# Kernel tuning notes

Hardware: AMD Instinct MI355X
Metric: run time of the kernel (lower is better)

## Reference

```python
import jax, jax.numpy as jnp
import numpy as np
import math

B, C, IMG, P = 32, 3, 224, 16
E, DEPTH, H, MLP = 768, 12, 12, 3072
NP = (IMG // P) ** 2          # 196 patches
S = NP + 1                    # 197 tokens with cls
NCLS = 10
HD = E // H                   # 64 head dim
EPS = 1e-5


def setup_inputs() -> dict:
    key = jax.random.key(0)
    ks = iter(jax.random.split(key, 64))
    n = lambda shape, s=0.02: (jax.random.normal(next(ks), shape, jnp.float32) * s)
    inp = {
        "x": jax.random.normal(next(ks), (B, C, IMG, IMG), jnp.float32),
        "conv_w": n((E, C, P, P)),
        "conv_b": jnp.zeros((E,), jnp.float32),
        "cls_token": n((1, 1, E)),
        "pos_embed": n((1, S, E)),
        # stacked per-layer params, leading dim DEPTH; linear weights stored [in, out]
        "ln1_w": jnp.ones((DEPTH, E), jnp.float32),
        "ln1_b": jnp.zeros((DEPTH, E), jnp.float32),
        "qkv_w": n((DEPTH, E, 3 * E)),
        "qkv_b": jnp.zeros((DEPTH, 3 * E), jnp.float32),
        "proj_w": n((DEPTH, E, E)),
        "proj_b": jnp.zeros((DEPTH, E), jnp.float32),
        "ln2_w": jnp.ones((DEPTH, E), jnp.float32),
        "ln2_b": jnp.zeros((DEPTH, E), jnp.float32),
        "mlp_w1": n((DEPTH, E, MLP)),
        "mlp_b1": jnp.zeros((DEPTH, MLP), jnp.float32),
        "mlp_w2": n((DEPTH, MLP, E)),
        "mlp_b2": jnp.zeros((DEPTH, E), jnp.float32),
        "lnf_w": jnp.ones((E,), jnp.float32),
        "lnf_b": jnp.zeros((E,), jnp.float32),
        "head_w": n((E, NCLS)),
        "head_b": jnp.zeros((NCLS,), jnp.float32),
    }
    return inp


def layernorm(x, w, b):
    mu = jnp.mean(x, axis=-1, keepdims=True)
    var = jnp.mean(jnp.square(x - mu), axis=-1, keepdims=True)
    return (x - mu) * jax.lax.rsqrt(var + EPS) * w + b


def reference(x, conv_w, conv_b, cls_token, pos_embed,
              ln1_w, ln1_b, qkv_w, qkv_b, proj_w, proj_b,
              ln2_w, ln2_b, mlp_w1, mlp_b1, mlp_w2, mlp_b2,
              lnf_w, lnf_b, head_w, head_b):
    # --- patch embedding: stride-P, kernel-P conv == patchify + matmul ---
    g = IMG // P  # 14
    patches = x.reshape(B, C, g, P, g, P).transpose(0, 2, 4, 1, 3, 5).reshape(B, NP, C * P * P)
    wp = conv_w.reshape(E, C * P * P)
    tok = jnp.einsum('bpd,ed->bpe', patches, wp) + conv_b  # [B, NP, E]

    # cls token + positional embedding (dropout = identity at eval)
    h = jnp.concatenate([jnp.broadcast_to(cls_token, (B, 1, E)), tok], axis=1) + pos_embed

    scale = math.sqrt(HD)
    for i in range(DEPTH):
        # --- attention ---
        y = layernorm(h, ln1_w[i], ln1_b[i])
        qkv = (y @ qkv_w[i] + qkv_b[i]).reshape(B, S, 3, H, HD)
        q, k, v = qkv[:, :, 0], qkv[:, :, 1], qkv[:, :, 2]  # [B, S, H, HD]
        attn = jnp.einsum('bqhd,bkhd->bhqk', q, k) / scale
        attn = jax.nn.softmax(attn, axis=-1)
        o = jnp.einsum('bhqk,bkhd->bqhd', attn, v).reshape(B, S, E)
        h = h + (o @ proj_w[i] + proj_b[i])
        # --- MLP ---
        y = layernorm(h, ln2_w[i], ln2_b[i])
        y = jax.nn.gelu(y @ mlp_w1[i] + mlp_b1[i], approximate=False)
        h = h + (y @ mlp_w2[i] + mlp_b2[i])

    h = layernorm(h, lnf_w, lnf_b)
    return h[:, 0] @ head_w + head_b  # [B, NCLS]
```

## Files before the change

### kernel.cpp

```cpp
#include <hip/hip_runtime.h>


typedef __attribute__((ext_vector_type(8))) short short8;
typedef __attribute__((ext_vector_type(8))) unsigned short ushort8;
typedef __attribute__((ext_vector_type(4))) float f32x4;
typedef unsigned short u16;

#define DEV __device__ __forceinline__

DEV u16 f2bf(float f) {
  unsigned int u = __builtin_bit_cast(unsigned int, f);
  u += 0x7fffu + ((u >> 16) & 1u);
  return (u16)(u >> 16);
}
DEV float wred_sum(float v) {
  for (int o = 32; o; o >>= 1) v += __shfl_xor(v, o, 64);
  return v;
}
DEV void glds16(const void* gp, void* lp) {
  __builtin_amdgcn_global_load_lds(
      (const __attribute__((address_space(1))) void*)gp,
      (__attribute__((address_space(3))) void*)lp, 16, 0, 0);
}
DEV int xcd_swz(int flat, int nwg) {
  int q = nwg >> 3, r = nwg & 7;
  int x = flat & 7, o = flat >> 3;
  return (x < r ? x * (q + 1) : r * (q + 1) + (x - r) * q) + o;
}

__global__ __launch_bounds__(256) void cvt4_k(const float* __restrict__ s,
                                              u16* __restrict__ d, long n4) {
  long i = (long)blockIdx.x * 256 + threadIdx.x;
  if (i >= n4) return;
  float4 v = ((const float4*)s)[i];
  ushort4 o;
  o.x = f2bf(v.x); o.y = f2bf(v.y); o.z = f2bf(v.z); o.w = f2bf(v.w);
  ((ushort4*)d)[i] = o;
}

__global__ __launch_bounds__(256) void tpose_k(const float* __restrict__ s,
                                               u16* __restrict__ d, int K,
                                               int N) {
  __shared__ float t[32][33];
  const int bx = blockIdx.x;
  const int by = blockIdx.y;
  const size_t base = (size_t)blockIdx.z * K * N;
  const int c = threadIdx.x & 31, r0 = threadIdx.x >> 5;
#pragma unroll
  for (int i = 0; i < 4; ++i) {
    int r = r0 + i * 8;
    t[r][c] = s[base + (size_t)(by * 32 + r) * N + bx * 32 + c];
  }
  __syncthreads();
#pragma unroll
  for (int i = 0; i < 4; ++i) {
    int r = r0 + i * 8;
    d[base + (size_t)(bx * 32 + r) * K + by * 32 + c] = f2bf(t[c][r]);
  }
}

__global__ __launch_bounds__(256) void patch_k(const float* __restrict__ x,
                                               u16* __restrict__ pt) {
  int i = blockIdx.x * 256 + threadIdx.x;
  int d = i % 768;
  int bp = i / 768;
  int p = bp % 196, b = bp / 196;
  int c = d >> 8, pd = d & 255;
  int py = pd >> 4, px = pd & 15;
  int gy = p / 14, gx = p - gy * 14;
  size_t src = ((size_t)(b * 3 + c) * 224 + gy * 16 + py) * 224 + gx * 16 + px;
  pt[i] = f2bf(x[src]);
}

__global__ __launch_bounds__(256) void clspos_k(const float* __restrict__ cls,
                                                const float* __restrict__ pos,
                                                float* __restrict__ h) {
  int i = blockIdx.x * 256 + threadIdx.x;
  int b = i / 768, e = i - b * 768;
  h[(size_t)b * 197 * 768 + e] = cls[e] + pos[e];
}

template <int EPI>
DEV void epi_store(float v, int grow, int gcol, u16* outb, int ldo,
                   float* outf, const float* pos) {
  if constexpr (EPI == 0) {
    outb[(size_t)grow * ldo + gcol] = f2bf(v);
  } else if constexpr (EPI == 1) {
    float u = __expf(-1.5957691216f * (v + 0.044715f * v * v * v));
    outb[(size_t)grow * ldo + gcol] = f2bf(v / (1.f + u));
  } else if constexpr (EPI == 2) {
    outf[(size_t)grow * ldo + gcol] += v;
  } else {
    int b = grow / 196, p = grow - b * 196;
    outf[(size_t)(grow + b + 1) * 768 + gcol] =
        v + pos[(size_t)(p + 1) * 768 + gcol];
  }
}

template <int EPI>
__global__ __launch_bounds__(512) void gemmK64(
    const u16* __restrict__ A, int lda, const u16* __restrict__ Bt, int ldb,
    const float* __restrict__ bias, u16* __restrict__ outb, int ldo,
    float* __restrict__ outf, const float* __restrict__ pos, int M, int N,
    int K) {
  __shared__ __align__(16) u16 Ak[2][128 * 64];
  __shared__ __align__(16) u16 Bk[2][128 * 64];
  const int tid = threadIdx.x;
  const int lane = tid & 63, wid = tid >> 6;
  const int wm = wid >> 2, wn = wid & 3;
  const int lg = lane >> 4, lr = lane & 15;
  const int nwg = gridDim.x * gridDim.y;
  const int wg = xcd_swz(blockIdx.y * gridDim.x + blockIdx.x, nwg);
  const int tn = wg % gridDim.x, tm = wg / gridDim.x;

  const int r8 = lane >> 3, c8 = lane & 7;
  const int swc = (c8 ^ r8) << 3;
  const u16* aS = A + (size_t)(tm * 128 + wid * 16 + r8) * lda + swc;
  const u16* bS = Bt + (size_t)(tn * 128 + wid * 16 + r8) * ldb + swc;

  auto stage = [&](int buf, int kt) {
    const u16* ak = aS + kt * 64;
    const u16* bk = bS + kt * 64;
    u16* ad = &Ak[buf][wid * 1024];
    u16* bd = &Bk[buf][wid * 1024];
    glds16(ak, ad);
    glds16(ak + (size_t)8 * lda, ad + 512);
    glds16(bk, bd);
    glds16(bk + (size_t)8 * ldb, bd + 512);
  };

  f32x4 acc[4][2] = {};
  auto compute = [&](int buf) {
#pragma unroll
    for (int ks = 0; ks < 2; ++ks) {
      const int pc = (ks << 2) | lg;
      const int po = ((pc ^ (lr & 7)) << 3);
      short8 af[4], bf2[2];
#pragma unroll
      for (int i = 0; i < 4; ++i)
        af[i] = *(const short8*)(&Ak[buf][(wm * 64 + i * 16 + lr) * 64 + po]);
#pragma unroll
      for (int i = 0; i < 2; ++i)
        bf2[i] = *(const short8*)(&Bk[buf][(wn * 32 + i * 16 + lr) * 64 + po]);
#pragma unroll
      for (int mi = 0; mi < 4; ++mi)
#pragma unroll
        for (int ni = 0; ni < 2; ++ni)
          acc[mi][ni] = __builtin_amdgcn_mfma_f32_16x16x32_bf16(
              af[mi], bf2[ni], acc[mi][ni], 0, 0, 0);
    }
  };

  const int nk = K >> 6;
  int cur = 0;
  stage(0, 0);
  __syncthreads();
  for (int kt = 0; kt < nk - 1; ++kt) {
    stage(cur ^ 1, kt + 1);
    compute(cur);
    __syncthreads();
    cur ^= 1;
  }
  compute(cur);

#pragma unroll
  for (int mi = 0; mi < 4; ++mi)
#pragma unroll
    for (int ni = 0; ni < 2; ++ni)
#pragma unroll
      for (int r = 0; r < 4; ++r) {
        int grow = tm * 128 + wm * 64 + mi * 16 + lg * 4 + r;
        int gcol = tn * 128 + wn * 32 + ni * 16 + lr;
        if (grow < M)
          epi_store<EPI>(acc[mi][ni][r] + bias[gcol], grow, gcol, outb, ldo,
                         outf, pos);
      }
}

template <int EPI>
__global__ __launch_bounds__(512) void gemmW2(
    const u16* __restrict__ A, int lda, const u16* __restrict__ Bt, int ldb,
    const float* __restrict__ bias, u16* __restrict__ outb, int ldo,
    float* __restrict__ outf, int M, int K) {
  __shared__ __align__(16) u16 Ak[2][128 * 32];
  __shared__ __align__(16) u16 Bk[2][256 * 32];
  const int tid = threadIdx.x;
  const int lane = tid & 63, wid = tid >> 6;
  const int wm = wid >> 2, wn = wid & 3;
  const int lg = lane >> 4, lr = lane & 15;
  const int nwg = gridDim.x * gridDim.y;
  const int wg = xcd_swz(blockIdx.y * gridDim.x + blockIdx.x, nwg);
  const int tn = wg % gridDim.x, tm = wg / gridDim.x;
  const size_t koff = (EPI == 4) ? (size_t)blockIdx.z * K : 0;

  const int sr = lane >> 2;
  const int sc4 = (((lane & 3) ^ ((lane >> 3) & 3)) << 3);
  const u16* aSrc = A + (size_t)(tm * 128 + wid * 16 + sr) * lda + koff + sc4;
  const u16* bSrc = Bt + (size_t)(tn * 256 + wid * 32 + sr) * ldb + koff + sc4;
  const size_t bRow16 = (size_t)16 * ldb;

  auto stage = [&](int buf, int kt) {
    const u16* ak = aSrc + kt * 32;
    const u16* bk = bSrc + kt * 32;
    glds16(ak, &Ak[buf][wid * 16 * 32]);
    u16* bd = &Bk[buf][wid * 32 * 32];
    glds16(bk, bd);
    glds16(bk + bRow16, bd + 512);
  };

  const int rp = (lg ^ ((lr >> 1) & 3)) << 3;
  f32x4 acc[4][4] = {};
  auto compute = [&](int buf) {
    short8 af[4], bf[4];
#pragma unroll
    for (int i = 0; i < 4; ++i)
      af[i] = *(const short8*)(&Ak[buf][(wm * 64 + i * 16 + lr) * 32 + rp]);
#pragma unroll
    for (int i = 0; i < 4; ++i)
      bf[i] = *(const short8*)(&Bk[buf][(wn * 64 + i * 16 + lr) * 32 + rp]);
#pragma unroll
    for (int mi = 0; mi < 4; ++mi)
#pragma unroll
      for (int ni = 0; ni < 4; ++ni)
        acc[mi][ni] = __builtin_amdgcn_mfma_f32_16x16x32_bf16(
            af[mi], bf[ni], acc[mi][ni], 0, 0, 0);
  };

  const int nk = K >> 5;
  int cur = 0;
  stage(0, 0);
  __syncthreads();
  for (int kt = 0; kt < nk - 1; ++kt) {
    stage(cur ^ 1, kt + 1);
    compute(cur);
    __syncthreads();
    cur ^= 1;
  }
  compute(cur);

#pragma unroll
  for (int mi = 0; mi < 4; ++mi)
#pragma unroll
    for (int ni = 0; ni < 4; ++ni)
#pragma unroll
      for (int r = 0; r < 4; ++r) {
        int grow = tm * 128 + wm * 64 + mi * 16 + lg * 4 + r;
        int gcol = tn * 256 + wn * 64 + ni * 16 + lr;
        if (grow < M) {
          if constexpr (EPI == 4) {
            outf[(size_t)blockIdx.z * M * ldo + (size_t)grow * ldo + gcol] =
                acc[mi][ni][r];
          } else {
            epi_store<EPI>(acc[mi][ni][r] + bias[gcol], grow, gcol, outb, ldo,
                           outf, nullptr);
          }
        }
      }
}

__global__ __launch_bounds__(256) void redK(const float* __restrict__ Cp,
                                            const float* __restrict__ bias,
                                            float* __restrict__ h) {
  size_t i = ((size_t)blockIdx.x * 256 + threadIdx.x) * 4;
  float4 p0 = *(const float4*)(Cp + i);
  float4 p1 = *(const float4*)(Cp + 6304ull * 768 + i);
  float4 p2 = *(const float4*)(Cp + 2ull * 6304 * 768 + i);
  float4 hv = *(const float4*)(h + i);
  float4 bv = *(const float4*)(bias + (int)(i % 768));
  hv.x += p0.x + p1.x + p2.x + bv.x;
  hv.y += p0.y + p1.y + p2.y + bv.y;
  hv.z += p0.z + p1.z + p2.z + bv.z;
  hv.w += p0.w + p1.w + p2.w + bv.w;
  *(float4*)(h + i) = hv;
}

__global__ __launch_bounds__(256) void redln_k(
    const float* __restrict__ Cp, const float* __restrict__ bias,
    float* __restrict__ h, const float* __restrict__ lnw,
    const float* __restrict__ lnb, u16* __restrict__ y) {
  const int lane = threadIdx.x & 63, wv = threadIdx.x >> 6;
  const int r = blockIdx.x * 4 + wv;
  const size_t base = (size_t)r * 768;
  float4 a[3];
  float s = 0.f, q = 0.f;
#pragma unroll
  for (int i = 0; i < 3; ++i) {
    const int off = i * 256 + lane * 4;
    float4 hv = *(const float4*)(h + base + off);
    float4 p0 = *(const float4*)(Cp + base + off);
    float4 p1 = *(const float4*)(Cp + 6304ull * 768 + base + off);
    float4 p2 = *(const float4*)(Cp + 2ull * 6304 * 768 + base + off);
    float4 bv = *(const float4*)(bias + off);
    a[i].x = hv.x + p0.x + p1.x + p2.x + bv.x;
    a[i].y = hv.y + p0.y + p1.y + p2.y + bv.y;
    a[i].z = hv.z + p0.z + p1.z + p2.z + bv.z;
    a[i].w = hv.w + p0.w + p1.w + p2.w + bv.w;
    s += a[i].x + a[i].y + a[i].z + a[i].w;
    q += a[i].x * a[i].x + a[i].y * a[i].y + a[i].z * a[i].z +
         a[i].w * a[i].w;
  }
  s = wred_sum(s);
  q = wred_sum(q);
  float mu = s * (1.f / 768.f);
  float var = q * (1.f / 768.f) - mu * mu;
  float rs = rsqrtf(var + 1e-5f);
#pragma unroll
  for (int i = 0; i < 3; ++i) {
    const int off = i * 256 + lane * 4;
    *(float4*)(h + base + off) = a[i];
    float4 wv4 = *(const float4*)(lnw + off);
    float4 bv4 = *(const float4*)(lnb + off);
    ushort4 o;
    o.x = f2bf((a[i].x - mu) * rs * wv4.x + bv4.x);
    o.y = f2bf((a[i].y - mu) * rs * wv4.y + bv4.y);
    o.z = f2bf((a[i].z - mu) * rs * wv4.z + bv4.z);
    o.w = f2bf((a[i].w - mu) * rs * wv4.w + bv4.w);
    *(ushort4*)(y + base + off) = o;
  }
}

template <int EPI, int BM>
__global__ __launch_bounds__(256) void gemmP(
    const u16* __restrict__ A, int lda, const u16* __restrict__ Bt, int ldb,
    const float* __restrict__ bias, u16* __restrict__ outb, int ldo,
    float* __restrict__ outf, const float* __restrict__ pos, int M, int N,
    int K) {
  constexpr int MI = BM / 32;
  __shared__ __align__(16) u16 Ak[2][BM * 32];
  __shared__ __align__(16) u16 Bk[2][128 * 32];
  const int tid = threadIdx.x;
  const int lane = tid & 63, wid = tid >> 6;
  const int wm = wid >> 1, wn = wid & 1;
  const int lg = lane >> 4, lr = lane & 15;
  const int nwg = gridDim.x * gridDim.y;
  const int wg = xcd_swz(blockIdx.y * gridDim.x + blockIdx.x, nwg);
  const int tn = wg % gridDim.x, tm = wg / gridDim.x;

  const int sr = lane >> 2;
  const int sc4 = (((lane & 3) ^ ((lane >> 3) & 3)) << 3);
  const u16* aSrc = A + (size_t)(tm * BM + wid * (BM / 4) + sr) * lda + sc4;
  const u16* bSrc = Bt + (size_t)(tn * 128 + wid * 32 + sr) * ldb + sc4;
  const size_t aRow16 = (size_t)16 * lda, bRow16 = (size_t)16 * ldb;

  auto stage = [&](int buf, int kt) {
    const u16* ak = aSrc + kt * 32;
    const u16* bk = bSrc + kt * 32;
    u16* ad = &Ak[buf][wid * (BM / 4) * 32];
    u16* bd = &Bk[buf][wid * 1024];
    glds16(ak, ad);
    if constexpr (BM == 128) glds16(ak + aRow16, ad + 512);
    glds16(bk, bd);
    glds16(bk + bRow16, bd + 512);
  };

  const int rp = (lg ^ ((lr >> 1) & 3)) << 3;
  f32x4 acc[MI][4] = {};
  auto compute = [&](int buf) {
    short8 af[MI], bfr[4];
#pragma unroll
    for (int i = 0; i < MI; ++i)
      af[i] =
          *(const short8*)(&Ak[buf][(wm * (BM / 2) + i * 16 + lr) * 32 + rp]);
#pragma unroll
    for (int i = 0; i < 4; ++i)
      bfr[i] = *(const short8*)(&Bk[buf][(wn * 64 + i * 16 + lr) * 32 + rp]);
#pragma unroll
    for (int mi = 0; mi < MI; ++mi)
#pragma unroll
      for (int ni = 0; ni < 4; ++ni)
        acc[mi][ni] = __builtin_amdgcn_mfma_f32_16x16x32_bf16(
            af[mi], bfr[ni], acc[mi][ni], 0, 0, 0);
  };

  const int nk = K >> 5;
  int cur = 0;
  stage(0, 0);
  __syncthreads();
  for (int kt = 0; kt < nk - 1; ++kt) {
    stage(cur ^ 1, kt + 1);
    compute(cur);
    __syncthreads();
    cur ^= 1;
  }
  compute(cur);

#pragma unroll
  for (int mi = 0; mi < MI; ++mi)
#pragma unroll
    for (int ni = 0; ni < 4; ++ni)
#pragma unroll
      for (int r = 0; r < 4; ++r) {
        int grow = tm * BM + wm * (BM / 2) + mi * 16 + lg * 4 + r;
        int gcol = tn * 128 + wn * 64 + ni * 16 + lr;
        if (grow < M)
          epi_store<EPI>(acc[mi][ni][r] + bias[gcol], grow, gcol, outb, ldo,
                         outf, pos);
      }
}

__global__ __launch_bounds__(64) void qksm_k(const u16* __restrict__ qkv,
                                             u16* __restrict__ P) {
  const int bh = blockIdx.x;
  const int qt = blockIdx.y;
  const int lane = threadIdx.x;
  const int lg = lane >> 4, lr = lane & 15;
  const int b = bh / 12, hh = bh - b * 12;
  const u16* base = qkv + (size_t)b * 197 * 2304 + hh * 64;
  int qrow = qt * 16 + lr;
  if (qrow > 196) qrow = 196;
  const u16* qp = base + (size_t)qrow * 2304 + lg * 8;
  short8 a0 = *(const short8*)(qp);
  short8 a1 = *(const short8*)(qp + 32);
  f32x4 c[13];
  const bool kval[2] = {true, (12 * 16 + lr) <= 196};
#pragma unroll
  for (int kt = 0; kt < 13; ++kt) {
    int krow = kt * 16 + lr;
    if (krow > 196) krow = 196;
    const u16* kp = base + 768 + (size_t)krow * 2304 + lg * 8;
    short8 b0 = *(const short8*)(kp);
    short8 b1 = *(const short8*)(kp + 32);
    f32x4 t = {0.f, 0.f, 0.f, 0.f};
    t = __builtin_amdgcn_mfma_f32_16x16x32_bf16(a0, b0, t, 0, 0, 0);
    c[kt] = __builtin_amdgcn_mfma_f32_16x16x32_bf16(a1, b1, t, 0, 0, 0);
  }
  float mr[4], sr_[4];
#pragma unroll
  for (int r = 0; r < 4; ++r) {
    float mm = -3.4e38f;
#pragma unroll
    for (int kt = 0; kt < 13; ++kt)
      if (kval[kt == 12]) mm = fmaxf(mm, c[kt][r] * 0.125f);
#pragma unroll
    for (int o = 1; o < 16; o <<= 1) mm = fmaxf(mm, __shfl_xor(mm, o, 64));
    mr[r] = mm;
  }
#pragma unroll
  for (int r = 0; r < 4; ++r) {
    float s = 0.f;
#pragma unroll
    for (int kt = 0; kt < 13; ++kt) {
      float e = kval[kt == 12] ? __expf(c[kt][r] * 0.125f - mr[r]) : 0.f;
      c[kt][r] = e;
      s += e;
    }
#pragma unroll
    for (int o = 1; o < 16; o <<= 1) s += __shfl_xor(s, o, 64);
    sr_[r] = 1.0f / s;
  }
  u16* pb = P + (size_t)bh * 197 * 224;
#pragma unroll
  for (int r = 0; r < 4; ++r) {
    int q = qt * 16 + lg * 4 + r;
    if (q < 197) {
#pragma unroll
      for (int kt = 0; kt < 13; ++kt)
        pb[(size_t)q * 224 + kt * 16 + lr] = f2bf(c[kt][r] * sr_[r]);
      pb[(size_t)q * 224 + 208 + lr] = 0;
    }
  }
}

__global__ __launch_bounds__(256) void pv_k(const u16* __restrict__ qkv,
                                            const u16* __restrict__ P,
                                            u16* __restrict__ o) {
  __shared__ __align__(16) u16 Vs[224 * 64];
  const int bh = blockIdx.x;
  const int b = bh / 12, hh = bh - b * 12;
  const int tid = threadIdx.x;
  const int lane = tid & 63, ct = tid >> 6;
  const int lg = lane >> 4, lr = lane & 15;
  const u16* vhead = qkv + (size_t)b * 197 * 2304 + 1536 + hh * 64;
#pragma unroll
  for (int it = 0; it < 7; ++it) {
    const int c0 = it * 256 + ct * 64;
    const int c = c0 + lane;
    int row = c >> 3;
    if (row > 196) row = 196;
    glds16(vhead + (size_t)row * 2304 + (c & 7) * 8, &Vs[c0 * 8]);
  }
  __syncthreads();
  short8 vf[7];
#pragma unroll
  for (int ks = 0; ks < 7; ++ks) {
    ushort8 t;
#pragma unroll
    for (int j = 0; j < 8; ++j) {
      int kk = ks * 32 + lg * 8 + j;
      t[j] = Vs[kk * 64 + ct * 16 + lr];
    }
    vf[ks] = __builtin_bit_cast(short8, t);
  }
  const u16* pbase = P + (size_t)bh * 197 * 224;
  u16* ob = o + (size_t)b * 197 * 768 + hh * 64 + ct * 16;
  for (int qt = 0; qt < 13; ++qt) {
    int q = qt * 16 + lr;
    if (q > 196) q = 196;
    const u16* pp = pbase + (size_t)q * 224 + lg * 8;
    f32x4 acc = {0.f, 0.f, 0.f, 0.f};
#pragma unroll
    for (int ks = 0; ks < 7; ++ks) {
      short8 af = *(const short8*)(pp + ks * 32);
      acc = __builtin_amdgcn_mfma_f32_16x16x32_bf16(af, vf[ks], acc, 0, 0, 0);
    }
#pragma unroll
    for (int r = 0; r < 4; ++r) {
      int qq = qt * 16 + lg * 4 + r;
      if (qq < 197) ob[(size_t)qq * 768 + lr] = f2bf(acc[r]);
    }
  }
}

__global__ __launch_bounds__(256) void ln_k(const float* __restrict__ x,
                                            const float* __restrict__ w,
                                            const float* __restrict__ bb,
                                            u16* __restrict__ y) {
  const int lane = threadIdx.x & 63, wv = threadIdx.x >> 6;
  const int r = blockIdx.x * 4 + wv;
  const float* xr = x + (size_t)r * 768;
  float4 v[3];
  float s = 0.f, q = 0.f;
#pragma unroll
  for (int i = 0; i < 3; ++i) {
    v[i] = *(const float4*)(xr + i * 256 + lane * 4);
    s += v[i].x + v[i].y + v[i].z + v[i].w;
    q += v[i].x * v[i].x + v[i].y * v[i].y + v[i].z * v[i].z +
         v[i].w * v[i].w;
  }
  s = wred_sum(s);
  q = wred_sum(q);
  float mu = s * (1.f / 768.f);
  float var = q * (1.f / 768.f) - mu * mu;
  float rs = rsqrtf(var + 1e-5f);
  u16* yr = y + (size_t)r * 768;
#pragma unroll
  for (int i = 0; i < 3; ++i) {
    float4 wv4 = *(const float4*)(w + i * 256 + lane * 4);
    float4 bv4 = *(const float4*)(bb + i * 256 + lane * 4);
    ushort4 o;
    o.x = f2bf((v[i].x - mu) * rs * wv4.x + bv4.x);
    o.y = f2bf((v[i].y - mu) * rs * wv4.y + bv4.y);
    o.z = f2bf((v[i].z - mu) * rs * wv4.z + bv4.z);
    o.w = f2bf((v[i].w - mu) * rs * wv4.w + bv4.w);
    *(ushort4*)(yr + i * 256 + lane * 4) = o;
  }
}

__global__ __launch_bounds__(256) void head_k(
    const float* __restrict__ h, const float* __restrict__ lnw,
    const float* __restrict__ lnb, const float* __restrict__ hw,
    const float* __restrict__ hb, float* __restrict__ out) {
  const int b = blockIdx.x, tid = threadIdx.x;
  const float* xr = h + (size_t)b * 197 * 768;
  float v0 = xr[tid], v1 = xr[tid + 256], v2 = xr[tid + 512];
  float s = v0 + v1 + v2;
  float q = v0 * v0 + v1 * v1 + v2 * v2;
  s = wred_sum(s);
  q = wred_sum(q);
  __shared__ float ss[4], qs[4];
  int lane = tid & 63, wid = tid >> 6;
  if (lane == 0) { ss[wid] = s; qs[wid] = q; }
  __syncthreads();
  float S = ss[0] + ss[1] + ss[2] + ss[3];
  float Q = qs[0] + qs[1] + qs[2] + qs[3];
  float mu = S * (1.f / 768.f);
  float var = Q * (1.f / 768.f) - mu * mu;
  float rs = rsqrtf(var + 1e-5f);
  __shared__ float yb[768];
  yb[tid] = (v0 - mu) * rs * lnw[tid] + lnb[tid];
  yb[tid + 256] = (v1 - mu) * rs * lnw[tid + 256] + lnb[tid + 256];
  yb[tid + 512] = (v2 - mu) * rs * lnw[tid + 512] + lnb[tid + 512];
  __syncthreads();
  float p[10] = {};
  for (int e = tid; e < 768; e += 256) {
    float yv = yb[e];
#pragma unroll
    for (int n = 0; n < 10; ++n) p[n] += yv * hw[(size_t)e * 10 + n];
  }
#pragma unroll
  for (int n = 0; n < 10; ++n) p[n] = wred_sum(p[n]);
  __shared__ float red[4][10];
  if (lane == 0)
#pragma unroll
    for (int n = 0; n < 10; ++n) red[wid][n] = p[n];
  __syncthreads();
  if (tid < 10)
    out[b * 10 + tid] =
        red[0][tid] + red[1][tid] + red[2][tid] + red[3][tid] + hb[tid];
}

extern "C" void kernel_launch(void* const* d_in, const int* in_sizes, int n_in,
                              void* d_out, int out_size, void* d_ws,
                              size_t ws_size, hipStream_t stream) {
  const float* x = (const float*)d_in[0];
  const float* conv_w = (const float*)d_in[1];
  const float* conv_b = (const float*)d_in[2];
  const float* cls = (const float*)d_in[3];
  const float* pos = (const float*)d_in[4];
  const float* ln1w = (const float*)d_in[5];
  const float* ln1b = (const float*)d_in[6];
  const float* qkvw = (const float*)d_in[7];
  const float* qkvbias = (const float*)d_in[8];
  const float* projw = (const float*)d_in[9];
  const float* projb = (const float*)d_in[10];
  const float* ln2w = (const float*)d_in[11];
  const float* ln2b = (const float*)d_in[12];
  const float* w1f = (const float*)d_in[13];
  const float* b1 = (const float*)d_in[14];
  const float* w2f = (const float*)d_in[15];
  const float* b2 = (const float*)d_in[16];
  const float* lnfw = (const float*)d_in[17];
  const float* lnfb = (const float*)d_in[18];
  const float* headw = (const float*)d_in[19];
  const float* headb = (const float*)d_in[20];
  float* out = (float*)d_out;

  char* p = (char*)d_ws;
  auto take = [&](size_t bytes) {
    char* q = p;
    p += (bytes + 255) & ~(size_t)255;
    return q;
  };
  u16* wq = (u16*)take(12ull * 768 * 2304 * 2);
  u16* wpj = (u16*)take(12ull * 768 * 768 * 2);
  u16* w1 = (u16*)take(12ull * 768 * 3072 * 2);
  u16* w2 = (u16*)take(12ull * 3072 * 768 * 2);
  u16* wc = (u16*)take(768ull * 768 * 2);
  float* h = (float*)take(6304ull * 768 * 4);
  u16* y = (u16*)take(6400ull * 768 * 2);
  u16* qkv = (u16*)take(6400ull * 2304 * 2);
  u16* ob = (u16*)take(6400ull * 768 * 2);
  u16* mlpb = (u16*)take(6400ull * 3072 * 2);
  u16* P = (u16*)take(384ull * 197 * 224 * 2);
  float* skP = (float*)take(3ull * 6304 * 768 * 4);
  (void)ws_size; (void)in_sizes; (void)n_in; (void)out_size;

  tpose_k<<<dim3(72, 24, 12), 256, 0, stream>>>(qkvw, wq, 768, 2304);
  tpose_k<<<dim3(24, 24, 12), 256, 0, stream>>>(projw, wpj, 768, 768);
  tpose_k<<<dim3(96, 24, 12), 256, 0, stream>>>(w1f, w1, 768, 3072);
  tpose_k<<<dim3(24, 96, 12), 256, 0, stream>>>(w2f, w2, 3072, 768);
  cvt4_k<<<576, 256, 0, stream>>>(conv_w, wc, 768 * 768 / 4);

  patch_k<<<6272 * 768 / 256, 256, 0, stream>>>(x, mlpb);
  gemmP<3, 64><<<dim3(6, 98), 256, 0, stream>>>(mlpb, 768, wc, 768, conv_b,
                                                nullptr, 0, h, pos, 6272, 768,
                                                768);
  clspos_k<<<32 * 768 / 256, 256, 0, stream>>>(cls, pos, h);

  ln_k<<<1576, 256, 0, stream>>>(h, ln1w, ln1b, y);
  for (int i = 0; i < 12; ++i) {
    gemmW2<0><<<dim3(9, 50), 512, 0, stream>>>(
        y, 768, wq + (size_t)i * 768 * 2304, 768, qkvbias + i * 2304, qkv,
        2304, nullptr, 6304, 768);
    qksm_k<<<dim3(384, 13), 64, 0, stream>>>(qkv, P);
    pv_k<<<384, 256, 0, stream>>>(qkv, P, ob);
    gemmP<2, 64><<<dim3(6, 99), 256, 0, stream>>>(
        ob, 768, wpj + (size_t)i * 768 * 768, 768, projb + i * 768, nullptr,
        768, h, nullptr, 6304, 768, 768);
    ln_k<<<1576, 256, 0, stream>>>(h, ln2w + i * 768, ln2b + i * 768, y);
    gemmK64<1><<<dim3(24, 50), 512, 0, stream>>>(
        y, 768, w1 + (size_t)i * 768 * 3072, 768, b1 + i * 3072, mlpb, 3072,
        nullptr, nullptr, 6304, 3072, 768);
    gemmW2<4><<<dim3(3, 50, 3), 512, 0, stream>>>(
        mlpb, 3072, w2 + (size_t)i * 3072 * 768, 3072, nullptr, nullptr, 768,
        skP, 6304, 1024);
    if (i < 11) {
      redln_k<<<1576, 256, 0, stream>>>(skP, b2 + i * 768, h,
                                        ln1w + (i + 1) * 768,
                                        ln1b + (i + 1) * 768, y);
    } else {
      redK<<<4728, 256, 0, stream>>>(skP, b2 + i * 768, h);
    }
  }

  head_k<<<32, 256, 0, stream>>>(h, lnfw, lnfb, headw, headb, out);
}
```

Before: 2.951 ms.

## Store split-K partials in bf16 and share K tile in LDS for QK softmax

The MLP down-projection split-K partial sums are now written as bf16 instead of fp32, and the reduction and LayerNorm kernels convert them back. This halves the traffic of the partial buffer, at the cost of bf16 rounding on each partial before the residual add. Separately, the QK-softmax kernel now uses one 256-thread block per batch-head. That block loads K into swizzled LDS once and loops its four waves over the query tiles, instead of every 64-thread block reloading K from global memory.

```diff
diff --git a/kernel.cpp b/kernel.cpp
--- a/kernel.cpp
+++ b/kernel.cpp
@@ -12,6 +12,9 @@
   unsigned int u = __builtin_bit_cast(unsigned int, f);
   u += 0x7fffu + ((u >> 16) & 1u);
   return (u16)(u >> 16);
+}
+DEV float bf2f(u16 v) {
+  return __builtin_bit_cast(float, (unsigned int)v << 16);
 }
 DEV float wred_sum(float v) {
   for (int o = 32; o; o >>= 1) v += __shfl_xor(v, o, 64);
@@ -248,8 +251,8 @@
         int gcol = tn * 256 + wn * 64 + ni * 16 + lr;
         if (grow < M) {
           if constexpr (EPI == 4) {
-            outf[(size_t)blockIdx.z * M * ldo + (size_t)grow * ldo + gcol] =
-                acc[mi][ni][r];
+            outb[(size_t)blockIdx.z * M * ldo + (size_t)grow * ldo + gcol] =
+                f2bf(acc[mi][ni][r]);
           } else {
             epi_store<EPI>(acc[mi][ni][r] + bias[gcol], grow, gcol, outb, ldo,
                            outf, nullptr);
@@ -258,24 +261,24 @@
       }
 }
 
-__global__ __launch_bounds__(256) void redK(const float* __restrict__ Cp,
+__global__ __launch_bounds__(256) void redK(const u16* __restrict__ Cp,
                                             const float* __restrict__ bias,
                                             float* __restrict__ h) {
   size_t i = ((size_t)blockIdx.x * 256 + threadIdx.x) * 4;
-  float4 p0 = *(const float4*)(Cp + i);
-  float4 p1 = *(const float4*)(Cp + 6304ull * 768 + i);
-  float4 p2 = *(const float4*)(Cp + 2ull * 6304 * 768 + i);
+  ushort4 q0 = *(const ushort4*)(Cp + i);
+  ushort4 q1 = *(const ushort4*)(Cp + 6304ull * 768 + i);
+  ushort4 q2 = *(const ushort4*)(Cp + 2ull * 6304 * 768 + i);
   float4 hv = *(const float4*)(h + i);
   float4 bv = *(const float4*)(bias + (int)(i % 768));
-  hv.x += p0.x + p1.x + p2.x + bv.x;
-  hv.y += p0.y + p1.y + p2.y + bv.y;
-  hv.z += p0.z + p1.z + p2.z + bv.z;
-  hv.w += p0.w + p1.w + p2.w + bv.w;
+  hv.x += bf2f(q0.x) + bf2f(q1.x) + bf2f(q2.x) + bv.x;
+  hv.y += bf2f(q0.y) + bf2f(q1.y) + bf2f(q2.y) + bv.y;
+  hv.z += bf2f(q0.z) + bf2f(q1.z) + bf2f(q2.z) + bv.z;
+  hv.w += bf2f(q0.w) + bf2f(q1.w) + bf2f(q2.w) + bv.w;
   *(float4*)(h + i) = hv;
 }
 
 __global__ __launch_bounds__(256) void redln_k(
-    const float* __restrict__ Cp, const float* __restrict__ bias,
+    const u16* __restrict__ Cp, const float* __restrict__ bias,
     float* __restrict__ h, const float* __restrict__ lnw,
     const float* __restrict__ lnb, u16* __restrict__ y) {
   const int lane = threadIdx.x & 63, wv = threadIdx.x >> 6;
@@ -287,14 +290,14 @@
   for (int i = 0; i < 3; ++i) {
     const int off = i * 256 + lane * 4;
     float4 hv = *(const float4*)(h + base + off);
-    float4 p0 = *(const float4*)(Cp + base + off);
-    float4 p1 = *(const float4*)(Cp + 6304ull * 768 + base + off);
-    float4 p2 = *(const float4*)(Cp + 2ull * 6304 * 768 + base + off);
+    ushort4 q0 = *(const ushort4*)(Cp + base + off);
+    ushort4 q1 = *(const ushort4*)(Cp + 6304ull * 768 + base + off);
+    ushort4 q2 = *(const ushort4*)(Cp + 2ull * 6304 * 768 + base + off);
     float4 bv = *(const float4*)(bias + off);
-    a[i].x = hv.x + p0.x + p1.x + p2.x + bv.x;
-    a[i].y = hv.y + p0.y + p1.y + p2.y + bv.y;
-    a[i].z = hv.z + p0.z + p1.z + p2.z + bv.z;
-    a[i].w = hv.w + p0.w + p1.w + p2.w + bv.w;
+    a[i].x = hv.x + bf2f(q0.x) + bf2f(q1.x) + bf2f(q2.x) + bv.x;
+    a[i].y = hv.y + bf2f(q0.y) + bf2f(q1.y) + bf2f(q2.y) + bv.y;
+    a[i].z = hv.z + bf2f(q0.z) + bf2f(q1.z) + bf2f(q2.z) + bv.z;
+    a[i].w = hv.w + bf2f(q0.w) + bf2f(q1.w) + bf2f(q2.w) + bv.w;
     s += a[i].x + a[i].y + a[i].z + a[i].w;
     q += a[i].x * a[i].x + a[i].y * a[i].y + a[i].z * a[i].z +
          a[i].w * a[i].w;
@@ -398,65 +401,80 @@
       }
 }
 
-__global__ __launch_bounds__(64) void qksm_k(const u16* __restrict__ qkv,
-                                             u16* __restrict__ P) {
+__global__ __launch_bounds__(256) void qksm_k(const u16* __restrict__ qkv,
+                                              u16* __restrict__ P) {
+  __shared__ __align__(16) u16 Ks[224 * 64];
   const int bh = blockIdx.x;
-  const int qt = blockIdx.y;
-  const int lane = threadIdx.x;
+  const int tid = threadIdx.x;
+  const int lane = tid & 63, w = tid >> 6;
   const int lg = lane >> 4, lr = lane & 15;
   const int b = bh / 12, hh = bh - b * 12;
+  const u16* kbase = qkv + (size_t)b * 197 * 2304 + 768 + hh * 64;
+#pragma unroll
+  for (int it = 0; it < 7; ++it) {
+    const int c0 = it * 256 + w * 64;
+    const int c = c0 + lane;
+    const int rd = c >> 3, c8 = c & 7;
+    const int rc = rd > 196 ? 196 : rd;
+    glds16(kbase + (size_t)rc * 2304 + ((c8 ^ (rd & 7)) << 3), &Ks[c0 * 8]);
+  }
+  __syncthreads();
+
   const u16* base = qkv + (size_t)b * 197 * 2304 + hh * 64;
-  int qrow = qt * 16 + lr;
-  if (qrow > 196) qrow = 196;
-  const u16* qp = base + (size_t)qrow * 2304 + lg * 8;
-  short8 a0 = *(const short8*)(qp);
-  short8 a1 = *(const short8*)(qp + 32);
-  f32x4 c[13];
-  const bool kval[2] = {true, (12 * 16 + lr) <= 196};
-#pragma unroll
-  for (int kt = 0; kt < 13; ++kt) {
-    int krow = kt * 16 + lr;
-    if (krow > 196) krow = 196;
-    const u16* kp = base + 768 + (size_t)krow * 2304 + lg * 8;
-    short8 b0 = *(const short8*)(kp);
-    short8 b1 = *(const short8*)(kp + 32);
-    f32x4 t = {0.f, 0.f, 0.f, 0.f};
-    t = __builtin_amdgcn_mfma_f32_16x16x32_bf16(a0, b0, t, 0, 0, 0);
-    c[kt] = __builtin_amdgcn_mfma_f32_16x16x32_bf16(a1, b1, t, 0, 0, 0);
-  }
-  float mr[4], sr_[4];
-#pragma unroll
-  for (int r = 0; r < 4; ++r) {
-    float mm = -3.4e38f;
-#pragma unroll
-    for (int kt = 0; kt < 13; ++kt)
-      if (kval[kt == 12]) mm = fmaxf(mm, c[kt][r] * 0.125f);
-#pragma unroll
-    for (int o = 1; o < 16; o <<= 1) mm = fmaxf(mm, __shfl_xor(mm, o, 64));
-    mr[r] = mm;
-  }
-#pragma unroll
-  for (int r = 0; r < 4; ++r) {
-    float s = 0.f;
+  const bool kval12 = (12 * 16 + lr) <= 196;
+  for (int qt = w; qt < 13; qt += 4) {
+    int qrow = qt * 16 + lr;
+    if (qrow > 196) qrow = 196;
+    const u16* qp = base + (size_t)qrow * 2304 + lg * 8;
+    short8 a0 = *(const short8*)(qp);
+    short8 a1 = *(const short8*)(qp + 32);
+    f32x4 c[13];
 #pragma unroll
     for (int kt = 0; kt < 13; ++kt) {
-      float e = kval[kt == 12] ? __expf(c[kt][r] * 0.125f - mr[r]) : 0.f;
-      c[kt][r] = e;
-      s += e;
-    }
-#pragma unroll
-    for (int o = 1; o < 16; o <<= 1) s += __shfl_xor(s, o, 64);
-    sr_[r] = 1.0f / s;
-  }
-  u16* pb = P + (size_t)bh * 197 * 224;
-#pragma unroll
-  for (int r = 0; r < 4; ++r) {
-    int q = qt * 16 + lg * 4 + r;
-    if (q < 197) {
+      const int krow = kt * 16 + lr;
+      short8 b0 =
+          *(const short8*)(&Ks[krow * 64 + ((lg ^ (krow & 7)) << 3)]);
+      short8 b1 =
+          *(const short8*)(&Ks[krow * 64 + (((4 + lg) ^ (krow & 7)) << 3)]);
+      f32x4 t = {0.f, 0.f, 0.f, 0.f};
+      t = __builtin_amdgcn_mfma_f32_16x16x32_bf16(a0, b0, t, 0, 0, 0);
+      c[kt] = __builtin_amdgcn_mfma_f32_16x16x32_bf16(a1, b1, t, 0, 0, 0);
+    }
+    float mr[4], sr_[4];
+#pragma unroll
+    for (int r = 0; r < 4; ++r) {
+      float mm = -3.4e38f;
 #pragma unroll
       for (int kt = 0; kt < 13; ++kt)
-        pb[(size_t)q * 224 + kt * 16 + lr] = f2bf(c[kt][r] * sr_[r]);
-      pb[(size_t)q * 224 + 208 + lr] = 0;
+        if (kt < 12 || kval12) mm = fmaxf(mm, c[kt][r] * 0.125f);
+#pragma unroll
+      for (int o = 1; o < 16; o <<= 1) mm = fmaxf(mm, __shfl_xor(mm, o, 64));
+      mr[r] = mm;
+    }
+#pragma unroll
+    for (int r = 0; r < 4; ++r) {
+      float s = 0.f;
+#pragma unroll
+      for (int kt = 0; kt < 13; ++kt) {
+        float e =
+            (kt < 12 || kval12) ? __expf(c[kt][r] * 0.125f - mr[r]) : 0.f;
+        c[kt][r] = e;
+        s += e;
+      }
+#pragma unroll
+      for (int o = 1; o < 16; o <<= 1) s += __shfl_xor(s, o, 64);
+      sr_[r] = 1.0f / s;
+    }
+    u16* pb = P + (size_t)bh * 197 * 224;
+#pragma unroll
+    for (int r = 0; r < 4; ++r) {
+      int q = qt * 16 + lg * 4 + r;
+      if (q < 197) {
+#pragma unroll
+        for (int kt = 0; kt < 13; ++kt)
+          pb[(size_t)q * 224 + kt * 16 + lr] = f2bf(c[kt][r] * sr_[r]);
+        pb[(size_t)q * 224 + 208 + lr] = 0;
+      }
     }
   }
 }
@@ -632,7 +650,7 @@
   u16* ob = (u16*)take(6400ull * 768 * 2);
   u16* mlpb = (u16*)take(6400ull * 3072 * 2);
   u16* P = (u16*)take(384ull * 197 * 224 * 2);
-  float* skP = (float*)take(3ull * 6304 * 768 * 4);
+  u16* skPb = (u16*)take(3ull * 6304 * 768 * 2);
   (void)ws_size; (void)in_sizes; (void)n_in; (void)out_size;
 
   tpose_k<<<dim3(72, 24, 12), 256, 0, stream>>>(qkvw, wq, 768, 2304);
@@ -652,7 +670,7 @@
     gemmW2<0><<<dim3(9, 50), 512, 0, stream>>>(
         y, 768, wq + (size_t)i * 768 * 2304, 768, qkvbias + i * 2304, qkv,
         2304, nullptr, 6304, 768);
-    qksm_k<<<dim3(384, 13), 64, 0, stream>>>(qkv, P);
+    qksm_k<<<384, 256, 0, stream>>>(qkv, P);
     pv_k<<<384, 256, 0, stream>>>(qkv, P, ob);
     gemmP<2, 64><<<dim3(6, 99), 256, 0, stream>>>(
         ob, 768, wpj + (size_t)i * 768 * 768, 768, projb + i * 768, nullptr,
@@ -662,14 +680,14 @@
         y, 768, w1 + (size_t)i * 768 * 3072, 768, b1 + i * 3072, mlpb, 3072,
         nullptr, nullptr, 6304, 3072, 768);
     gemmW2<4><<<dim3(3, 50, 3), 512, 0, stream>>>(
-        mlpb, 3072, w2 + (size_t)i * 3072 * 768, 3072, nullptr, nullptr, 768,
-        skP, 6304, 1024);
+        mlpb, 3072, w2 + (size_t)i * 3072 * 768, 3072, nullptr, skPb, 768,
+        nullptr, 6304, 1024);
     if (i < 11) {
-      redln_k<<<1576, 256, 0, stream>>>(skP, b2 + i * 768, h,
+      redln_k<<<1576, 256, 0, stream>>>(skPb, b2 + i * 768, h,
                                         ln1w + (i + 1) * 768,
                                         ln1b + (i + 1) * 768, y);
     } else {
-      redK<<<4728, 256, 0, stream>>>(skP, b2 + i * 768, h);
+      redK<<<4728, 256, 0, stream>>>(skPb, b2 + i * 768, h);
     }
   }
 
```

After: 2.841 ms. -3.7%, faster.
